# Optimization experiments

Hardware: AMD Instinct MI355X
Metric: run time of the kernel (lower is better)

Reference implementation:

```python
import jax, jax.numpy as jnp
import numpy as np

# DeepSeek-V3 style router hyperparameters (from init_kwargs)
N_EXPERTS = 256
N_GROUP = 8
TOPK_GROUP = 4
TOP_K = 8
ROUTED_SCALING_FACTOR = 2.5
NORM_TOPK_PROB = True


def setup_inputs() -> dict:
    key = jax.random.key(0)
    k1, k2, k3 = jax.random.split(key, 3)
    hidden_states = jax.random.normal(k1, (4, 4096, 7168), dtype=jnp.float32)
    weight = jax.random.normal(k2, (7168, N_EXPERTS), dtype=jnp.float32) * 0.02
    bias = jax.random.normal(k3, (N_EXPERTS,), dtype=jnp.float32) * 0.1
    return {"hidden_states": hidden_states, "weight": weight, "bias": bias}


def reference(hidden_states, weight, bias):
    bsz, seq_len, h = hidden_states.shape
    n_tok = bsz * seq_len
    x = hidden_states.reshape(n_tok, h).astype(jnp.float32)

    # gating linear + sigmoid scoring
    logits = jnp.einsum('nh,he->ne', x, weight.astype(jnp.float32))
    scores = jax.nn.sigmoid(logits)
    scores_for_choice = scores + bias[None, :]  # [n_tok, E]

    # hierarchical group top-k: group score = sum of top-2 experts in group
    e_per_g = N_EXPERTS // N_GROUP
    group_features = scores_for_choice.reshape(n_tok, N_GROUP, e_per_g)
    group_scores = jax.lax.top_k(group_features, 2)[0].sum(axis=-1)  # [n_tok, G]
    _, group_idx = jax.lax.top_k(group_scores, k=TOPK_GROUP)  # [n_tok, topk_group]

    # build group mask and broadcast to expert mask
    group_mask = jnp.zeros_like(group_scores)
    group_mask = group_mask.at[jnp.arange(n_tok)[:, None], group_idx].set(1.0)
    score_mask = jnp.broadcast_to(
        group_mask[..., None], (n_tok, N_GROUP, e_per_g)
    ).reshape(n_tok, N_EXPERTS)

    # expert top-k within selected groups
    tmp_scores = jnp.where(score_mask.astype(bool), scores_for_choice, 0.0)
    _, topk_idx = jax.lax.top_k(tmp_scores, k=TOP_K)  # [n_tok, top_k]
    topk_weight = jnp.take_along_axis(scores_for_choice, topk_idx, axis=-1)

    if TOP_K > 1 and NORM_TOPK_PROB:
        denominator = topk_weight.sum(axis=-1, keepdims=True) + 1e-20
        topk_weight = topk_weight / denominator
    topk_weight = topk_weight * ROUTED_SCALING_FACTOR
    return topk_idx, topk_weight
```

## Files before the change

kernel.cpp:

```cpp
#include <hip/hip_runtime.h>
#include <math.h>

#define KDIM   7168
#define NEXP   256
#define NTOK   16384
#define KSTEPS 224

typedef _Float16 half8 __attribute__((ext_vector_type(8)));
typedef _Float16 half4 __attribute__((ext_vector_type(4)));
typedef float    f32x4 __attribute__((ext_vector_type(4)));

__global__ __launch_bounds__(256, 1) void split_w(
    const float* __restrict__ W, _Float16* __restrict__ wh, _Float16* __restrict__ wl)
{
  const int n  = threadIdx.x;
  const int ks = blockIdx.x >> 2;
  const int kc = blockIdx.x & 3;
  const int kb = ks * 32 + kc * 8;
  half8 hv, lv;
#pragma unroll
  for (int i = 0; i < 8; ++i) {
    const float x = W[(size_t)(kb + i) * NEXP + n] * 1024.0f;
    const _Float16 h = (_Float16)x;
    hv[i] = h;
    lv[i] = (_Float16)(x - (float)h);
  }
  const size_t o = ((((size_t)ks * 16 + (n >> 4)) * 4 + kc) * 16 + (n & 15)) * 8;
  *(half8*)(wh + o) = hv;
  *(half8*)(wl + o) = lv;
}

__global__ __launch_bounds__(512, 2) void gemm_route(
    const float* __restrict__ A,
    const _Float16* __restrict__ Wh,
    const _Float16* __restrict__ Wl,
    const float* __restrict__ bias,
    float* __restrict__ out_idx,
    float* __restrict__ out_w)
{
  __shared__ _Float16 a_hi[64 * 32];
  __shared__ _Float16 a_lo[64 * 32];
  __shared__ float    s_rows[64][256];

  const int tid = threadIdx.x;
  const int wv  = tid >> 6;
  const int ln  = tid & 63;
  const int m0  = blockIdx.x << 6;

  const int sm = tid >> 3;
  const int sk = (tid & 7) << 2;
  const float* Ap = A + (size_t)(m0 + sm) * KDIM + sk;
  const int soff = (((sm >> 4) * 4 + (sk >> 3)) * 16 + (sm & 15)) * 8 + (sk & 7);

  const size_t bo0 = (size_t)(wv * 2 + 0) * 512 + (size_t)ln * 8;
  const size_t bo1 = (size_t)(wv * 2 + 1) * 512 + (size_t)ln * 8;

  f32x4 acc[4][2];
#pragma unroll
  for (int i = 0; i < 4; ++i) {
    f32x4 z = {0.f, 0.f, 0.f, 0.f};
    acc[i][0] = z; acc[i][1] = z;
  }

  float4 pa  = *(const float4*)Ap;
  half8 nbh0 = *(const half8*)(Wh + bo0);
  half8 nbh1 = *(const half8*)(Wh + bo1);
  half8 nbl0 = *(const half8*)(Wl + bo0);
  half8 nbl1 = *(const half8*)(Wl + bo1);

  for (int ks = 0; ks < KSTEPS; ++ks) {
    const float x0 = pa.x * 1024.f, x1 = pa.y * 1024.f,
                x2 = pa.z * 1024.f, x3 = pa.w * 1024.f;
    const _Float16 h0 = (_Float16)x0, h1 = (_Float16)x1,
                   h2 = (_Float16)x2, h3 = (_Float16)x3;
    half4 hv = {h0, h1, h2, h3};
    half4 lv = {(_Float16)(x0 - (float)h0), (_Float16)(x1 - (float)h1),
                (_Float16)(x2 - (float)h2), (_Float16)(x3 - (float)h3)};

    __syncthreads();
    *(half4*)(&a_hi[soff]) = hv;
    *(half4*)(&a_lo[soff]) = lv;
    __syncthreads();

    const half8 bh0 = nbh0, bh1 = nbh1, bl0 = nbl0, bl1 = nbl1;
    if (ks + 1 < KSTEPS) {
      pa = *(const float4*)(Ap + (size_t)(ks + 1) * 32);
      const size_t adv = (size_t)(ks + 1) * 8192;
      nbh0 = *(const half8*)(Wh + adv + bo0);
      nbh1 = *(const half8*)(Wh + adv + bo1);
      nbl0 = *(const half8*)(Wl + adv + bo0);
      nbl1 = *(const half8*)(Wl + adv + bo1);
    }

#pragma unroll
    for (int mf = 0; mf < 4; ++mf) {
      const half8 ah = *(const half8*)(&a_hi[mf * 512 + ln * 8]);
      const half8 al = *(const half8*)(&a_lo[mf * 512 + ln * 8]);
      acc[mf][0] = __builtin_amdgcn_mfma_f32_16x16x32_f16(ah, bh0, acc[mf][0], 0, 0, 0);
      acc[mf][1] = __builtin_amdgcn_mfma_f32_16x16x32_f16(ah, bh1, acc[mf][1], 0, 0, 0);
      acc[mf][0] = __builtin_amdgcn_mfma_f32_16x16x32_f16(ah, bl0, acc[mf][0], 0, 0, 0);
      acc[mf][1] = __builtin_amdgcn_mfma_f32_16x16x32_f16(ah, bl1, acc[mf][1], 0, 0, 0);
      acc[mf][0] = __builtin_amdgcn_mfma_f32_16x16x32_f16(al, bh0, acc[mf][0], 0, 0, 0);
      acc[mf][1] = __builtin_amdgcn_mfma_f32_16x16x32_f16(al, bh1, acc[mf][1], 0, 0, 0);
    }
  }

  const int   fq = ln >> 4, fr = ln & 15;
  const float b0 = bias[wv * 32 + fr];
  const float b1 = bias[wv * 32 + 16 + fr];
  const float SC = 1.0f / 1048576.0f;
#pragma unroll
  for (int mf = 0; mf < 4; ++mf) {
#pragma unroll
    for (int j = 0; j < 4; ++j) {
      const int row = mf * 16 + fq * 4 + j;
      const int c0  = wv * 32 + fr;
      const int c1  = c0 + 16;
      s_rows[row][c0 ^ (row & 31)] = 1.0f / (1.0f + expf(-acc[mf][0][j] * SC)) + b0;
      s_rows[row][c1 ^ (row & 31)] = 1.0f / (1.0f + expf(-acc[mf][1][j] * SC)) + b1;
    }
  }
  __syncthreads();

  if (tid < 64) {
    const int sw = tid & 31;
    const float* row = &s_rows[tid][0];
#define RD(e) row[(e) ^ sw]
    float gs[8];
#pragma unroll
    for (int g = 0; g < 8; ++g) {
      float m1 = -3.0e38f, m2 = -3.0e38f;
#pragma unroll
      for (int e = 0; e < 32; ++e) {
        const float v = RD(g * 32 + e);
        if (v > m1) { m2 = m1; m1 = v; }
        else if (v > m2) { m2 = v; }
      }
      gs[g] = m1 + m2;
    }

    int selmask = 0;
#pragma unroll
    for (int k = 0; k < 4; ++k) {
      float best = -3.0e38f; int bg = 0;
#pragma unroll
      for (int g = 0; g < 8; ++g)
        if (!((selmask >> g) & 1) && gs[g] > best) { best = gs[g]; bg = g; }
      selmask |= (1 << bg);
    }

    float tv[8]; int ti[8];
#pragma unroll
    for (int i = 0; i < 8; ++i) { tv[i] = -3.0e38f; ti[i] = 0; }
#pragma unroll 4
    for (int e = 0; e < 256; ++e) {
      const bool sel = (selmask >> (e >> 5)) & 1;
      const float v = sel ? RD(e) : 0.0f;
      if (v > tv[7]) {
        tv[7] = v; ti[7] = e;
#pragma unroll
        for (int p = 7; p > 0; --p) {
          if (tv[p] > tv[p - 1]) {
            const float tf = tv[p]; tv[p] = tv[p - 1]; tv[p - 1] = tf;
            const int   tt = ti[p]; ti[p] = ti[p - 1]; ti[p - 1] = tt;
          }
        }
      }
    }

    float w8[8], denom = 0.f;
#pragma unroll
    for (int i = 0; i < 8; ++i) { w8[i] = RD(ti[i]); denom += w8[i]; }
    denom += 1e-20f;

    const size_t t = (size_t)m0 + tid;
#pragma unroll
    for (int i = 0; i < 8; ++i) {
      out_idx[t * 8 + i] = (float)ti[i];
      out_w[t * 8 + i]   = (w8[i] / denom) * 2.5f;
    }
#undef RD
  }
}

extern "C" void kernel_launch(void* const* d_in, const int* in_sizes, int n_in,
                              void* d_out, int out_size, void* d_ws, size_t ws_size,
                              hipStream_t stream)
{
  const float* hs   = (const float*)d_in[0];
  const float* w    = (const float*)d_in[1];
  const float* bias = (const float*)d_in[2];
  float* out = (float*)d_out;

  _Float16* wh = (_Float16*)d_ws;
  _Float16* wl = wh + (size_t)KDIM * NEXP;

  split_w<<<KSTEPS * 4, 256, 0, stream>>>(w, wh, wl);
  gemm_route<<<NTOK / 64, 512, 0, stream>>>(hs, wh, wl, bias, out, out + (size_t)NTOK * 8);
}
```

Before: 868.3 us.

## Retile router GEMM to 32-row blocks with 128-wide K steps and union LDS

Shrinks the M tile from 64 to 32 rows and widens each K iteration to 128, so there are four 32-wide sub-steps per pair of barriers instead of one. B fragments are now loaded directly inside the unrolled loop rather than register-prefetched. The A staging buffer and the score rows share one LDS union, and launch bounds move to 4 blocks per SM, so more blocks fit on each CU. The trade-off is that every block rereads the whole split weight matrix, which doubles total weight traffic, and weight loads are no longer prefetched ahead of use.

```diff
diff --git a/kernel.cpp b/kernel.cpp
--- a/kernel.cpp
+++ b/kernel.cpp
@@ -4,10 +4,11 @@
 #define KDIM   7168
 #define NEXP   256
 #define NTOK   16384
-#define KSTEPS 224
+#define BM     32
+#define BK     128
+#define NIT    (KDIM / BK)
 
 typedef _Float16 half8 __attribute__((ext_vector_type(8)));
-typedef _Float16 half4 __attribute__((ext_vector_type(4)));
 typedef float    f32x4 __attribute__((ext_vector_type(4)));
 
 __global__ __launch_bounds__(256, 1) void split_w(
@@ -30,7 +31,9 @@
   *(half8*)(wl + o) = lv;
 }
 
-__global__ __launch_bounds__(512, 2) void gemm_route(
+#define MFMA  __builtin_amdgcn_mfma_f32_16x16x32_f16
+
+__global__ __launch_bounds__(512, 4) void gemm_route(
     const float* __restrict__ A,
     const _Float16* __restrict__ Wh,
     const _Float16* __restrict__ Wl,
@@ -38,93 +41,97 @@
     float* __restrict__ out_idx,
     float* __restrict__ out_w)
 {
-  __shared__ _Float16 a_hi[64 * 32];
-  __shared__ _Float16 a_lo[64 * 32];
-  __shared__ float    s_rows[64][256];
+  __shared__ union {
+    _Float16 a[2][BM * BK];
+    float    rows[BM][256];
+  } sm;
 
   const int tid = threadIdx.x;
   const int wv  = tid >> 6;
   const int ln  = tid & 63;
-  const int m0  = blockIdx.x << 6;
-
-  const int sm = tid >> 3;
-  const int sk = (tid & 7) << 2;
-  const float* Ap = A + (size_t)(m0 + sm) * KDIM + sk;
-  const int soff = (((sm >> 4) * 4 + (sk >> 3)) * 16 + (sm & 15)) * 8 + (sk & 7);
-
-  const size_t bo0 = (size_t)(wv * 2 + 0) * 512 + (size_t)ln * 8;
-  const size_t bo1 = (size_t)(wv * 2 + 1) * 512 + (size_t)ln * 8;
-
-  f32x4 acc[4][2];
-#pragma unroll
-  for (int i = 0; i < 4; ++i) {
-    f32x4 z = {0.f, 0.f, 0.f, 0.f};
-    acc[i][0] = z; acc[i][1] = z;
-  }
-
-  float4 pa  = *(const float4*)Ap;
-  half8 nbh0 = *(const half8*)(Wh + bo0);
-  half8 nbh1 = *(const half8*)(Wh + bo1);
-  half8 nbl0 = *(const half8*)(Wl + bo0);
-  half8 nbl1 = *(const half8*)(Wl + bo1);
-
-  for (int ks = 0; ks < KSTEPS; ++ks) {
-    const float x0 = pa.x * 1024.f, x1 = pa.y * 1024.f,
-                x2 = pa.z * 1024.f, x3 = pa.w * 1024.f;
-    const _Float16 h0 = (_Float16)x0, h1 = (_Float16)x1,
-                   h2 = (_Float16)x2, h3 = (_Float16)x3;
-    half4 hv = {h0, h1, h2, h3};
-    half4 lv = {(_Float16)(x0 - (float)h0), (_Float16)(x1 - (float)h1),
-                (_Float16)(x2 - (float)h2), (_Float16)(x3 - (float)h3)};
-
+  const int m0  = blockIdx.x * BM;
+
+  const int srow = (((tid >> 6) & 1) << 4) | (tid & 15);
+  const int skol = ((tid >> 7) << 5) | (((tid >> 4) & 3) << 3);
+  const float* Ap = A + (size_t)(m0 + srow) * KDIM + skol;
+
+  const int boff = wv * 1024 + ln * 8;
+  const _Float16* Bh = Wh + boff;
+  const _Float16* Bl = Wl + boff;
+
+  f32x4 acc00 = {0.f, 0.f, 0.f, 0.f}, acc01 = acc00, acc10 = acc00, acc11 = acc00;
+
+  float4 pa0 = *(const float4*)(Ap);
+  float4 pa1 = *(const float4*)(Ap + 4);
+
+  for (int it = 0; it < NIT; ++it) {
     __syncthreads();
-    *(half4*)(&a_hi[soff]) = hv;
-    *(half4*)(&a_lo[soff]) = lv;
+    {
+      float xx[8] = {pa0.x, pa0.y, pa0.z, pa0.w, pa1.x, pa1.y, pa1.z, pa1.w};
+      half8 hv, lv;
+#pragma unroll
+      for (int q = 0; q < 8; ++q) {
+        const float xs = xx[q] * 1024.0f;
+        const _Float16 hh = (_Float16)xs;
+        hv[q] = hh;
+        lv[q] = (_Float16)(xs - (float)hh);
+      }
+      *(half8*)&sm.a[0][tid * 8] = hv;
+      *(half8*)&sm.a[1][tid * 8] = lv;
+    }
     __syncthreads();
 
-    const half8 bh0 = nbh0, bh1 = nbh1, bl0 = nbl0, bl1 = nbl1;
-    if (ks + 1 < KSTEPS) {
-      pa = *(const float4*)(Ap + (size_t)(ks + 1) * 32);
-      const size_t adv = (size_t)(ks + 1) * 8192;
-      nbh0 = *(const half8*)(Wh + adv + bo0);
-      nbh1 = *(const half8*)(Wh + adv + bo1);
-      nbl0 = *(const half8*)(Wl + adv + bo0);
-      nbl1 = *(const half8*)(Wl + adv + bo1);
-    }
-
-#pragma unroll
-    for (int mf = 0; mf < 4; ++mf) {
-      const half8 ah = *(const half8*)(&a_hi[mf * 512 + ln * 8]);
-      const half8 al = *(const half8*)(&a_lo[mf * 512 + ln * 8]);
-      acc[mf][0] = __builtin_amdgcn_mfma_f32_16x16x32_f16(ah, bh0, acc[mf][0], 0, 0, 0);
-      acc[mf][1] = __builtin_amdgcn_mfma_f32_16x16x32_f16(ah, bh1, acc[mf][1], 0, 0, 0);
-      acc[mf][0] = __builtin_amdgcn_mfma_f32_16x16x32_f16(ah, bl0, acc[mf][0], 0, 0, 0);
-      acc[mf][1] = __builtin_amdgcn_mfma_f32_16x16x32_f16(ah, bl1, acc[mf][1], 0, 0, 0);
-      acc[mf][0] = __builtin_amdgcn_mfma_f32_16x16x32_f16(al, bh0, acc[mf][0], 0, 0, 0);
-      acc[mf][1] = __builtin_amdgcn_mfma_f32_16x16x32_f16(al, bh1, acc[mf][1], 0, 0, 0);
-    }
-  }
-
+    if (it + 1 < NIT) {
+      pa0 = *(const float4*)(Ap + (size_t)(it + 1) * BK);
+      pa1 = *(const float4*)(Ap + (size_t)(it + 1) * BK + 4);
+    }
+
+#pragma unroll
+    for (int s = 0; s < 4; ++s) {
+      const int kadv = (it * 4 + s) * 8192;
+      const half8 bh0 = *(const half8*)(Bh + kadv);
+      const half8 bh1 = *(const half8*)(Bh + kadv + 512);
+      const half8 bl0 = *(const half8*)(Bl + kadv);
+      const half8 bl1 = *(const half8*)(Bl + kadv + 512);
+      const half8 ah0 = *(const half8*)&sm.a[0][s * 1024 + ln * 8];
+      const half8 ah1 = *(const half8*)&sm.a[0][s * 1024 + 512 + ln * 8];
+      const half8 al0 = *(const half8*)&sm.a[1][s * 1024 + ln * 8];
+      const half8 al1 = *(const half8*)&sm.a[1][s * 1024 + 512 + ln * 8];
+      acc00 = MFMA(ah0, bh0, acc00, 0, 0, 0);
+      acc01 = MFMA(ah0, bh1, acc01, 0, 0, 0);
+      acc10 = MFMA(ah1, bh0, acc10, 0, 0, 0);
+      acc11 = MFMA(ah1, bh1, acc11, 0, 0, 0);
+      acc00 = MFMA(ah0, bl0, acc00, 0, 0, 0);
+      acc01 = MFMA(ah0, bl1, acc01, 0, 0, 0);
+      acc10 = MFMA(ah1, bl0, acc10, 0, 0, 0);
+      acc11 = MFMA(ah1, bl1, acc11, 0, 0, 0);
+      acc00 = MFMA(al0, bh0, acc00, 0, 0, 0);
+      acc01 = MFMA(al0, bh1, acc01, 0, 0, 0);
+      acc10 = MFMA(al1, bh0, acc10, 0, 0, 0);
+      acc11 = MFMA(al1, bh1, acc11, 0, 0, 0);
+    }
+  }
+
+  __syncthreads();
   const int   fq = ln >> 4, fr = ln & 15;
-  const float b0 = bias[wv * 32 + fr];
-  const float b1 = bias[wv * 32 + 16 + fr];
-  const float SC = 1.0f / 1048576.0f;
-#pragma unroll
-  for (int mf = 0; mf < 4; ++mf) {
-#pragma unroll
-    for (int j = 0; j < 4; ++j) {
-      const int row = mf * 16 + fq * 4 + j;
-      const int c0  = wv * 32 + fr;
-      const int c1  = c0 + 16;
-      s_rows[row][c0 ^ (row & 31)] = 1.0f / (1.0f + expf(-acc[mf][0][j] * SC)) + b0;
-      s_rows[row][c1 ^ (row & 31)] = 1.0f / (1.0f + expf(-acc[mf][1][j] * SC)) + b1;
-    }
+  const float b0v = bias[wv * 32 + fr];
+  const float b1v = bias[wv * 32 + 16 + fr];
+  const float SC  = 1.0f / 1048576.0f;
+  const int   c0  = wv * 32 + fr, c1 = c0 + 16;
+#pragma unroll
+  for (int j = 0; j < 4; ++j) {
+    const int r0 = fq * 4 + j;
+    const int r1 = 16 + fq * 4 + j;
+    sm.rows[r0][c0 ^ (r0 & 31)] = 1.0f / (1.0f + expf(-acc00[j] * SC)) + b0v;
+    sm.rows[r0][c1 ^ (r0 & 31)] = 1.0f / (1.0f + expf(-acc01[j] * SC)) + b1v;
+    sm.rows[r1][c0 ^ (r1 & 31)] = 1.0f / (1.0f + expf(-acc10[j] * SC)) + b0v;
+    sm.rows[r1][c1 ^ (r1 & 31)] = 1.0f / (1.0f + expf(-acc11[j] * SC)) + b1v;
   }
   __syncthreads();
 
-  if (tid < 64) {
+  if (tid < 32) {
     const int sw = tid & 31;
-    const float* row = &s_rows[tid][0];
+    const float* row = &sm.rows[tid][0];
 #define RD(e) row[(e) ^ sw]
     float gs[8];
 #pragma unroll
@@ -195,6 +202,6 @@
   _Float16* wh = (_Float16*)d_ws;
   _Float16* wl = wh + (size_t)KDIM * NEXP;
 
-  split_w<<<KSTEPS * 4, 256, 0, stream>>>(w, wh, wl);
-  gemm_route<<<NTOK / 64, 512, 0, stream>>>(hs, wh, wl, bias, out, out + (size_t)NTOK * 8);
+  split_w<<<896, 256, 0, stream>>>(w, wh, wl);
+  gemm_route<<<NTOK / BM, 512, 0, stream>>>(hs, wh, wl, bias, out, out + (size_t)NTOK * 8);
 }
```

After: 856.1 us. No clear change (-1.4%).
